# Performance work log

Measured on AMD Instinct MI355X. Metric: run time of the kernel, lower is better.

The kernel has to match this reference:

```python
import jax, jax.numpy as jnp
import numpy as np
import math

H = 512       # hidden_dim
NL = 4        # num_layers
N2 = 32       # d_state // 2
B, L = 8, 4096
DT_MIN, DT_MAX = 1e-3, 1e-1
EPS = 1e-5


def _layer_norm(x, gamma, beta):
    mu = jnp.mean(x, axis=-1, keepdims=True)
    var = jnp.mean(jnp.square(x - mu), axis=-1, keepdims=True)
    return (x - mu) * jax.lax.rsqrt(var + EPS) * gamma + beta


def setup_inputs() -> dict:
    key = jax.random.key(0)
    ks = jax.random.split(key, 8)
    x = jax.random.normal(ks[0], (B, L, H), dtype=jnp.float32)
    # S4DKernel buffers / params, stacked over layers
    log_dt = jax.random.uniform(ks[1], (NL, H)) * (math.log(DT_MAX) - math.log(DT_MIN)) + math.log(DT_MIN)
    A_imag = jnp.broadcast_to(math.pi * jnp.arange(N2, dtype=jnp.float32), (NL, H, N2)).copy()
    log_A_real = jnp.full((NL, H, N2), math.log(0.5), dtype=jnp.float32)
    C = jax.random.normal(ks[2], (NL, H, N2, 2), dtype=jnp.float32)  # view_as_real of cfloat
    D = jax.random.normal(ks[3], (NL, H), dtype=jnp.float32)
    # 1x1 Conv1d h -> 2h (pointwise linear over channels)
    W = jax.random.normal(ks[4], (NL, 2 * H, H), dtype=jnp.float32) / math.sqrt(H)
    b = jax.random.normal(ks[5], (NL, 2 * H), dtype=jnp.float32) * 0.01
    gamma = jnp.ones((NL, H), dtype=jnp.float32)
    beta = jnp.zeros((NL, H), dtype=jnp.float32)
    return dict(x=x, log_dt=log_dt, A_imag=A_imag, log_A_real=log_A_real,
                C=C, D=D, W=W, b=b, gamma=gamma, beta=beta)


def reference(x, log_dt, A_imag, log_A_real, C, D, W, b, gamma, beta):
    Bsz, Lseq, h = x.shape
    t = jnp.arange(Lseq, dtype=jnp.float32)
    for i in range(NL):
        # --- S4D kernel generation ---
        dt = jnp.exp(log_dt[i])                                    # (h,)
        Cc = C[i, ..., 0] + 1j * C[i, ..., 1]                      # (h, n)
        A = -jnp.exp(log_A_real[i]) + 1j * A_imag[i]               # (h, n)
        dA = A * dt[:, None]                                       # (h, n)
        Cmod = Cc * (jnp.exp(dA) - 1.0) / A                        # (h, n)
        # Vandermonde: exp(dA * l), reduced over state dim
        K = 2.0 * jnp.einsum('hn,hnl->hl', Cmod,
                             jnp.exp(dA[:, :, None] * t)).real     # (h, L)
        # --- FFT long convolution ---
        u = jnp.transpose(x, (0, 2, 1))                            # (B, h, L)
        kf = jnp.fft.rfft(K, n=2 * Lseq)                           # (h, L+1)
        uf = jnp.fft.rfft(u, n=2 * Lseq)                           # (B, h, L+1)
        y = jnp.fft.irfft(uf * kf, n=2 * Lseq)[..., :Lseq]         # (B, h, L)
        y = y + u * D[i][:, None]
        y = jax.nn.gelu(y, approximate=False)                      # torch nn.GELU default (erf)
        # 1x1 conv h -> 2h then GLU over channel dim
        z = jnp.einsum('oh,bhl->bol', W[i], y) + b[i][None, :, None]
        a, g = jnp.split(z, 2, axis=1)
        y = a * jax.nn.sigmoid(g)                                  # (B, h, L)
        y = jnp.transpose(y, (0, 2, 1))                            # (B, L, h)
        x = _layer_norm(y + x, gamma[i], beta[i])
    return x
```

## Files before the change

kernel.cpp:

```cpp
#include <hip/hip_runtime.h>
#include <hip/hip_bf16.h>
#include <math.h>

#define H 512
#define NL 4
#define N2 32
#define Bsz 8
#define Lseq 4096
#define BT (Bsz*Lseq)
#define LC2 64
#define NCC (BT/LC2)
#define CPB (Lseq/LC2)

typedef __attribute__((ext_vector_type(8))) short short8;
typedef __attribute__((ext_vector_type(4))) float float4v;


__device__ __forceinline__ float bf2f(unsigned short u) {
    union { unsigned int i; float f; } x; x.i = ((unsigned int)u) << 16; return x.f;
}
__device__ __forceinline__ unsigned short f2bf(float f) {
    union { float f; unsigned int i; } x; x.f = f;
    unsigned int u = x.i + 0x7fff + ((x.i >> 16) & 1);
    return (unsigned short)(u >> 16);
}
__device__ __forceinline__ uint2 pack4bf(float a, float b, float c, float d) {
    uint2 r;
    r.x = (unsigned)f2bf(a) | ((unsigned)f2bf(b) << 16);
    r.y = (unsigned)f2bf(c) | ((unsigned)f2bf(d) << 16);
    return r;
}
__device__ __forceinline__ void async_copy16(const void* g, void* l) {
    __builtin_amdgcn_global_load_lds(
        (const __attribute__((address_space(1))) void*)g,
        (__attribute__((address_space(3))) void*)l, 16, 0, 0);
}

__global__ void wconv_kernel(const float* __restrict__ W, unsigned short* __restrict__ Wbf) {
    int tid = blockIdx.x * 256 + threadIdx.x;
    Wbf[tid] = f2bf(W[tid]);
}

__global__ void params_kernel(const float* __restrict__ log_dt, const float* __restrict__ A_imag,
                              const float* __restrict__ log_A_real, const float* __restrict__ Cin,
                              float* __restrict__ dA, float* __restrict__ Ct) {
    int tid = blockIdx.x * 256 + threadIdx.x;
    int h = tid % H;
    int n = (tid / H) % N2;
    int layer = tid / (H * N2);
    float dt = expf(log_dt[layer * H + h]);
    int pidx = (layer * H + h) * N2 + n;
    float Are = -expf(log_A_real[pidx]);
    float Aim = A_imag[pidx];
    float dre = Are * dt, dim = Aim * dt;
    float er = expf(dre);
    float lre = er * cosf(dim), lim = er * sinf(dim);
    float nre = lre - 1.0f, nim = lim;
    float inv = 1.0f / (Are * Are + Aim * Aim);
    float tre = (nre * Are + nim * Aim) * inv;
    float tim = (nim * Are - nre * Aim) * inv;
    float Ccre = Cin[pidx * 2], Ccim = Cin[pidx * 2 + 1];
    int oidx = ((layer * N2 + n) * 2) * H + h;
    dA[oidx] = dre;  dA[oidx + H] = dim;
    Ct[oidx] = 2.0f * (Ccre * tre - Ccim * tim);
    Ct[oidx + H] = 2.0f * (Ccre * tim + Ccim * tre);
}

__global__ void kergen_k_kernel(const float* __restrict__ dA, const float* __restrict__ Ct,
                                unsigned short* __restrict__ kmat) {
    int t = blockIdx.x * 256 + threadIdx.x;
    int d = t & 63;
    int h = (t >> 6) & (H - 1);
    int layer = t >> 15;
    float fd = (float)d;
    float sum = 0.f;
    for (int n = 0; n < N2; n++) {
        int base = ((layer * N2 + n) * 2) * H + h;
        float dre = dA[base], dim = dA[base + H];
        float Ctr = Ct[base], Cti = Ct[base + H];
        float e = expf(dre * fd);
        sum += Ctr * e * cosf(dim * fd) - Cti * e * sinf(dim * fd);
    }
    kmat[t] = f2bf(sum);
}

__global__ void kergenW_kernel(const float* __restrict__ dA, unsigned short* __restrict__ Wst, int layer) {
    int t = blockIdx.x * 256 + threadIdx.x;
    int j = t & 63;
    int r = (t >> 6) & 63;
    int h = t >> 12;
    int n = r >> 1;
    int base = ((layer * N2 + n) * 2) * H + h;
    float dre = dA[base], dim = dA[base + H];
    float p = (float)(63 - j);
    float e = expf(dre * p);
    Wst[t] = f2bf((r & 1) ? e * sinf(dim * p) : e * cosf(dim * p));
}

__global__ void kergenV_kernel(const float* __restrict__ dA, const float* __restrict__ Ct,
                               unsigned short* __restrict__ Vl, int layer) {
    int t = blockIdx.x * 256 + threadIdx.x;
    int c2 = t & 63;
    int l = (t >> 6) & 63;
    int h = t >> 12;
    int n = c2 >> 1;
    int base = ((layer * N2 + n) * 2) * H + h;
    float dre = dA[base], dim = dA[base + H];
    float Ctr = Ct[base], Cti = Ct[base + H];
    float q = (float)(l + 1);
    float e = expf(dre * q);
    float ar = e * cosf(dim * q), ai = e * sinf(dim * q);
    float vre = Ctr * ar - Cti * ai;
    float vim = Ctr * ai + Cti * ar;
    Vl[t] = f2bf((c2 & 1) ? -vim : vre);
}

__global__ __launch_bounds__(256) void t1_f32_kernel(const float* __restrict__ xi,
                                                     unsigned short* __restrict__ ut) {
    __shared__ float tile[64][68];
    int bx = blockIdx.x;
    int pt = bx & 511, ht = bx >> 9;
    int p0 = pt * 64, h0 = ht * 64;
    int t = threadIdx.x;
    int jr = t & 15, ib = t >> 4;
#pragma unroll
    for (int pass = 0; pass < 4; pass++) {
        int i = ib + pass * 16;
        float4 v = *(const float4*)(xi + (size_t)(p0 + i) * H + h0 + jr * 4);
        tile[i][jr * 4 + 0] = v.x; tile[i][jr * 4 + 1] = v.y;
        tile[i][jr * 4 + 2] = v.z; tile[i][jr * 4 + 3] = v.w;
    }
    __syncthreads();
#pragma unroll
    for (int pass = 0; pass < 4; pass++) {
        int i2 = ib + pass * 16;
        int j2 = jr * 4;
        uint2 pk = pack4bf(tile[j2][i2], tile[j2 + 1][i2], tile[j2 + 2][i2], tile[j2 + 3][i2]);
        *(uint2*)(ut + (size_t)(h0 + i2) * BT + p0 + j2) = pk;
    }
}

__global__ __launch_bounds__(256) void t1_bf16_kernel(const unsigned short* __restrict__ xi,
                                                      unsigned short* __restrict__ ut) {
    __shared__ unsigned short tile[64][72];
    int bx = blockIdx.x;
    int pt = bx & 511, ht = bx >> 9;
    int p0 = pt * 64, h0 = ht * 64;
    int t = threadIdx.x;
    int jr = t & 7, ib = t >> 3;
#pragma unroll
    for (int pass = 0; pass < 2; pass++) {
        int i = ib + pass * 32;
        short8 v = *reinterpret_cast<const short8*>(xi + (size_t)(p0 + i) * H + h0 + jr * 8);
#pragma unroll
        for (int e = 0; e < 8; e++) tile[i][jr * 8 + e] = (unsigned short)v[e];
    }
    __syncthreads();
    int hr = t >> 2, bg = t & 3;
    short8 o0, o1;
#pragma unroll
    for (int r = 0; r < 8; r++) o0[r] = (short)tile[bg * 16 + r][hr];
#pragma unroll
    for (int r = 0; r < 8; r++) o1[r] = (short)tile[bg * 16 + 8 + r][hr];
    unsigned short* dst = ut + (size_t)(h0 + hr) * BT + p0 + bg * 16;
    *reinterpret_cast<short8*>(dst) = o0;
    *reinterpret_cast<short8*>(dst + 8) = o1;
}

__global__ __launch_bounds__(256) void states_kernel(const unsigned short* __restrict__ ut,
                                                     const unsigned short* __restrict__ Wst,
                                                     unsigned short* __restrict__ Sloc) {
    int h = blockIdx.x;
    int wave = threadIdx.x >> 6, lane = threadIdx.x & 63;
    int r16 = lane & 15, quad = lane >> 4;
    const unsigned short* uh = ut + (size_t)h * BT;
    const unsigned short* wh = Wst + (size_t)h * 64 * 64;
    unsigned short* sh = Sloc + (size_t)h * NCC * 64;
    for (int nt = 0; nt < 8; nt++) {
        int cc0 = wave * 128 + nt * 16;
        float4v acc[4] = {};
#pragma unroll
        for (int k0 = 0; k0 < 64; k0 += 32) {
            short8 bf = *reinterpret_cast<const short8*>(uh + (size_t)(cc0 + r16) * 64 + k0 + quad * 8);
#pragma unroll
            for (int mt = 0; mt < 4; mt++) {
                short8 af = *reinterpret_cast<const short8*>(wh + (mt * 16 + r16) * 64 + k0 + quad * 8);
                acc[mt] = __builtin_amdgcn_mfma_f32_16x16x32_bf16(af, bf, acc[mt], 0, 0, 0);
            }
        }
        int cc = cc0 + r16;
#pragma unroll
        for (int mt = 0; mt < 4; mt++) {
            uint2 pk = pack4bf(acc[mt][0], acc[mt][1], acc[mt][2], acc[mt][3]);
            *(uint2*)(sh + (size_t)cc * 64 + mt * 16 + quad * 4) = pk;
        }
    }
}

__global__ void combine_kernel(unsigned short* __restrict__ Sloc, const float* __restrict__ dA, int layer) {
    int t = blockIdx.x * 256 + threadIdx.x;
    int n = t & 31;
    int b = (t >> 5) & 7;
    int h = t >> 8;
    int base = ((layer * N2 + n) * 2) * H + h;
    float dre = dA[base], dim = dA[base + H];
    float e = expf(dre * 64.f);
    float Lr = e * cosf(dim * 64.f), Li = e * sinf(dim * 64.f);
    unsigned int* p = (unsigned int*)Sloc + ((size_t)h * NCC + b * CPB) * 32 + n;
    float sr = 0.f, si = 0.f;
    for (int c = 0; c < CPB; c++) {
        unsigned int v = p[(size_t)c * 32];
        float pr = bf2f(v & 0xffff), pi = bf2f(v >> 16);
        p[(size_t)c * 32] = (unsigned)f2bf(sr) | ((unsigned)f2bf(si) << 16);
        float nr = fmaf(Lr, sr, fmaf(-Li, si, pr));
        float ni = fmaf(Lr, si, fmaf(Li, sr, pi));
        sr = nr; si = ni;
    }
}

__global__ __launch_bounds__(256) void conv_kernel(const unsigned short* __restrict__ ut,
                                                   const unsigned short* __restrict__ kmat,
                                                   const unsigned short* __restrict__ Vl,
                                                   const unsigned short* __restrict__ Sent,
                                                   const float* __restrict__ Dp,
                                                   unsigned short* __restrict__ yt, int layer) {
    __shared__ unsigned short T[64][72];
    int h = blockIdx.x, half = blockIdx.y;
    int t = threadIdx.x;
    const unsigned short* km = kmat + ((size_t)layer * H + h) * 64;
    {
        int l = t >> 2, j0 = (t & 3) * 16;
#pragma unroll
        for (int g = 0; g < 2; g++) {
            short8 v;
#pragma unroll
            for (int e = 0; e < 8; e++) {
                int j = j0 + g * 8 + e;
                v[e] = (j <= l) ? (short)km[l - j] : (short)0;
            }
            *reinterpret_cast<short8*>(&T[l][j0 + g * 8]) = v;
        }
    }
    __syncthreads();
    int wave = t >> 6, lane = t & 63;
    int r16 = lane & 15, quad = lane >> 4;
    const unsigned short* uh = ut + (size_t)h * BT;
    const unsigned short* vh = Vl + (size_t)h * 64 * 64;
    const unsigned short* eh = Sent + (size_t)h * NCC * 64;
    unsigned short* yh = yt + (size_t)h * BT;
    float Dh = Dp[layer * H + h];
    for (int nt = 0; nt < 4; nt++) {
        int cc0 = half * 256 + wave * 64 + nt * 16;
        float4v acc[4] = {};
#pragma unroll
        for (int k0 = 0; k0 < 64; k0 += 32) {
            short8 bf = *reinterpret_cast<const short8*>(uh + (size_t)(cc0 + r16) * 64 + k0 + quad * 8);
#pragma unroll
            for (int mt = 0; mt < 4; mt++) {
                short8 af = *reinterpret_cast<const short8*>(&T[mt * 16 + r16][k0 + quad * 8]);
                acc[mt] = __builtin_amdgcn_mfma_f32_16x16x32_bf16(af, bf, acc[mt], 0, 0, 0);
            }
        }
#pragma unroll
        for (int k0 = 0; k0 < 64; k0 += 32) {
            short8 bf = *reinterpret_cast<const short8*>(eh + (size_t)(cc0 + r16) * 64 + k0 + quad * 8);
#pragma unroll
            for (int mt = 0; mt < 4; mt++) {
                short8 af = *reinterpret_cast<const short8*>(vh + (mt * 16 + r16) * 64 + k0 + quad * 8);
                acc[mt] = __builtin_amdgcn_mfma_f32_16x16x32_bf16(af, bf, acc[mt], 0, 0, 0);
            }
        }
        int cc = cc0 + r16;
#pragma unroll
        for (int mt = 0; mt < 4; mt++) {
            size_t p = (size_t)cc * 64 + mt * 16 + quad * 4;
            ushort4 uu = *(const ushort4*)(uh + p);
            float o[4];
#pragma unroll
            for (int r = 0; r < 4; r++) {
                float y = acc[mt][r] + Dh * bf2f(((const unsigned short*)&uu)[r]);
                o[r] = 0.5f * y * (1.0f + erff(y * 0.70710678118654752f));
            }
            *(uint2*)(yh + p) = pack4bf(o[0], o[1], o[2], o[3]);
        }
    }
}

__global__ __launch_bounds__(256) void transpose2_kernel(const unsigned short* __restrict__ yt,
                                                         unsigned short* __restrict__ yb) {
    __shared__ unsigned short tile[64][72];
    int bx = blockIdx.x;
    int pt = bx & 511, ht = bx >> 9;
    int p0 = pt * 64, h0 = ht * 64;
    int t = threadIdx.x;
    int jr = t & 7, ib = t >> 3;
#pragma unroll
    for (int pass = 0; pass < 2; pass++) {
        int i = ib + pass * 32;
        short8 v = *reinterpret_cast<const short8*>(yt + (size_t)(h0 + i) * BT + p0 + jr * 8);
#pragma unroll
        for (int e = 0; e < 8; e++) tile[i][jr * 8 + e] = (unsigned short)v[e];
    }
    __syncthreads();
    int pp = t >> 2, hg = t & 3;
    short8 o0, o1;
#pragma unroll
    for (int r = 0; r < 8; r++) o0[r] = (short)tile[hg * 16 + r][pp];
#pragma unroll
    for (int r = 0; r < 8; r++) o1[r] = (short)tile[hg * 16 + 8 + r][pp];
    unsigned short* dst = yb + (size_t)(p0 + pp) * H + h0 + hg * 16;
    *reinterpret_cast<short8*>(dst) = o0;
    *reinterpret_cast<short8*>(dst + 8) = o1;
}

__global__ __launch_bounds__(256) void gemm_glu_kernel(const unsigned short* __restrict__ ybf,
                                                       const unsigned short* __restrict__ Wbf,
                                                       const float* __restrict__ bias,
                                                       unsigned short* __restrict__ yo, int layer) {
    __shared__ unsigned short As[128 * 32];
    __shared__ unsigned short Bs[128 * 32];
    int tid = threadIdx.x;
    int wave = tid >> 6, lane = tid & 63;
    int wr = wave >> 1, wc = wave & 1;
    int r16 = lane & 15, quad = lane >> 4;
    int m0 = blockIdx.x * 128;
    int o0 = blockIdx.y * 64;
    const unsigned short* Wl = Wbf + (size_t)layer * 2 * H * H;

    int srow = lane >> 2;
    int scol = ((lane & 3) ^ ((srow >> 1) & 3)) * 8;
    const unsigned short* aSrc0 = ybf + ((size_t)(m0 + wave * 16 + srow)) * H + scol;
    const unsigned short* aSrc1 = aSrc0 + (size_t)64 * H;
    const unsigned short* bSrcA = Wl + ((size_t)(o0 + wave * 16 + srow)) * H + scol;
    const unsigned short* bSrcG = bSrcA + (size_t)512 * H;
    unsigned short* aDst0 = As + (wave * 16) * 32;
    unsigned short* aDst1 = As + (64 + wave * 16) * 32;
    unsigned short* bDstA = Bs + (wave * 16) * 32;
    unsigned short* bDstG = Bs + (64 + wave * 16) * 32;

    int rcol = (quad ^ ((r16 >> 1) & 3)) * 8;

    float4v acc_a[4][2] = {}, acc_g[4][2] = {};

    for (int k0 = 0; k0 < H; k0 += 32) {
        __syncthreads();
        async_copy16(aSrc0, aDst0);
        async_copy16(aSrc1, aDst1);
        async_copy16(bSrcA, bDstA);
        async_copy16(bSrcG, bDstG);
        aSrc0 += 32; aSrc1 += 32; bSrcA += 32; bSrcG += 32;
        __syncthreads();

        short8 af[4], ba[2], bg[2];
#pragma unroll
        for (int mi = 0; mi < 4; mi++)
            af[mi] = *reinterpret_cast<const short8*>(As + (wr * 64 + mi * 16 + r16) * 32 + rcol);
#pragma unroll
        for (int ni = 0; ni < 2; ni++) {
            ba[ni] = *reinterpret_cast<const short8*>(Bs + (wc * 32 + ni * 16 + r16) * 32 + rcol);
            bg[ni] = *reinterpret_cast<const short8*>(Bs + (64 + wc * 32 + ni * 16 + r16) * 32 + rcol);
        }
#pragma unroll
        for (int mi = 0; mi < 4; mi++)
#pragma unroll
            for (int ni = 0; ni < 2; ni++) {
                acc_a[mi][ni] = __builtin_amdgcn_mfma_f32_16x16x32_bf16(af[mi], ba[ni], acc_a[mi][ni], 0, 0, 0);
                acc_g[mi][ni] = __builtin_amdgcn_mfma_f32_16x16x32_bf16(af[mi], bg[ni], acc_g[mi][ni], 0, 0, 0);
            }
    }

    const float* bl = bias + layer * 2 * H;
#pragma unroll
    for (int ni = 0; ni < 2; ni++) {
        int o = o0 + wc * 32 + ni * 16 + r16;
        float ba_ = bl[o], bg_ = bl[H + o];
#pragma unroll
        for (int mi = 0; mi < 4; mi++)
#pragma unroll
            for (int r = 0; r < 4; r++) {
                int l = m0 + wr * 64 + mi * 16 + quad * 4 + r;
                float av = acc_a[mi][ni][r] + ba_;
                float gv = acc_g[mi][ni][r] + bg_;
                yo[(size_t)l * H + o] = f2bf(av * (1.0f / (1.0f + expf(-gv))));
            }
    }
}

__global__ __launch_bounds__(256) void ln_kernel(const unsigned short* __restrict__ yo,
                                                 const float* __restrict__ xf,
                                                 const unsigned short* __restrict__ xb,
                                                 const float* __restrict__ gamma, const float* __restrict__ beta,
                                                 float* __restrict__ of, unsigned short* __restrict__ ob,
                                                 int in_f32, int out_f32, int layer) {
    int wave = threadIdx.x >> 6, lane = threadIdx.x & 63;
    size_t row = (size_t)blockIdx.x * 4 + wave;
    const unsigned short* yp = yo + row * H + lane * 8;
    short8 yv = *reinterpret_cast<const short8*>(yp);
    float v[8];
    if (in_f32) {
        const float* xp = xf + row * H + lane * 8;
        float4 x0 = *(const float4*)(xp);
        float4 x1 = *(const float4*)(xp + 4);
        v[0] = bf2f((unsigned short)yv[0]) + x0.x; v[1] = bf2f((unsigned short)yv[1]) + x0.y;
        v[2] = bf2f((unsigned short)yv[2]) + x0.z; v[3] = bf2f((unsigned short)yv[3]) + x0.w;
        v[4] = bf2f((unsigned short)yv[4]) + x1.x; v[5] = bf2f((unsigned short)yv[5]) + x1.y;
        v[6] = bf2f((unsigned short)yv[6]) + x1.z; v[7] = bf2f((unsigned short)yv[7]) + x1.w;
    } else {
        const unsigned short* xp = xb + row * H + lane * 8;
        short8 xv = *reinterpret_cast<const short8*>(xp);
#pragma unroll
        for (int i = 0; i < 8; i++)
            v[i] = bf2f((unsigned short)yv[i]) + bf2f((unsigned short)xv[i]);
    }
    float s = 0.f, s2 = 0.f;
#pragma unroll
    for (int i = 0; i < 8; i++) { s += v[i]; s2 = fmaf(v[i], v[i], s2); }
#pragma unroll
    for (int off = 32; off; off >>= 1) {
        s += __shfl_xor(s, off);
        s2 += __shfl_xor(s2, off);
    }
    float mu = s * (1.0f / H);
    float var = s2 * (1.0f / H) - mu * mu;
    float inv = rsqrtf(var + 1e-5f);
    const float* gl = gamma + layer * H + lane * 8;
    const float* bl = beta + layer * H + lane * 8;
    float o[8];
#pragma unroll
    for (int i = 0; i < 8; i++)
        o[i] = (v[i] - mu) * inv * gl[i] + bl[i];
    if (out_f32) {
        float* op = of + row * H + lane * 8;
        *(float4*)(op) = make_float4(o[0], o[1], o[2], o[3]);
        *(float4*)(op + 4) = make_float4(o[4], o[5], o[6], o[7]);
    } else {
        unsigned short* op = ob + row * H + lane * 8;
        uint2 p0 = pack4bf(o[0], o[1], o[2], o[3]);
        uint2 p1 = pack4bf(o[4], o[5], o[6], o[7]);
        *(uint2*)(op) = p0;
        *(uint2*)(op + 4) = p1;
    }
}

extern "C" void kernel_launch(void* const* d_in, const int* in_sizes, int n_in,
                              void* d_out, int out_size, void* d_ws, size_t ws_size,
                              hipStream_t stream) {
    const float* x          = (const float*)d_in[0];
    const float* log_dt     = (const float*)d_in[1];
    const float* A_imag     = (const float*)d_in[2];
    const float* log_A_real = (const float*)d_in[3];
    const float* C          = (const float*)d_in[4];
    const float* D          = (const float*)d_in[5];
    const float* W          = (const float*)d_in[6];
    const float* bias       = (const float*)d_in[7];
    const float* gamma      = (const float*)d_in[8];
    const float* beta       = (const float*)d_in[9];

    char* ws = (char*)d_ws;
    unsigned short* xR   = (unsigned short*)(ws + 0);
    unsigned short* Sloc = (unsigned short*)(ws + 67108864);
    unsigned short* u_t  = (unsigned short*)(ws + 100663296);
    unsigned short* ybf  = (unsigned short*)(ws + 100663296);
    unsigned short* y_t  = (unsigned short*)(ws + 134217728);
    unsigned short* yo   = (unsigned short*)(ws + 134217728);
    unsigned short* Wbf  = (unsigned short*)(ws + 167772160);
    unsigned short* WV   = (unsigned short*)(ws + 171966464);
    unsigned short* kmat = (unsigned short*)(ws + 176160768);
    float*          dA   = (float*)(ws + 176422912);
    float*          Ct   = (float*)(ws + 176947200);
    float* xout_final    = (float*)d_out;

    wconv_kernel<<<NL * 2 * H * H / 256, 256, 0, stream>>>(W, Wbf);
    params_kernel<<<NL * N2 * H / 256, 256, 0, stream>>>(log_dt, A_imag, log_A_real, C, dA, Ct);
    kergen_k_kernel<<<NL * H * 64 / 256, 256, 0, stream>>>(dA, Ct, kmat);

    for (int layer = 0; layer < NL; ++layer) {
        if (layer == 0)
            t1_f32_kernel<<<4096, 256, 0, stream>>>(x, u_t);
        else
            t1_bf16_kernel<<<4096, 256, 0, stream>>>(xR, u_t);
        kergenW_kernel<<<H * 64 * 64 / 256, 256, 0, stream>>>(dA, WV, layer);
        states_kernel<<<H, 256, 0, stream>>>(u_t, WV, Sloc);
        combine_kernel<<<H * Bsz * N2 / 256, 256, 0, stream>>>(Sloc, dA, layer);
        kergenV_kernel<<<H * 64 * 64 / 256, 256, 0, stream>>>(dA, Ct, WV, layer);
        conv_kernel<<<dim3(H, 2), 256, 0, stream>>>(u_t, kmat, WV, Sloc, D, y_t, layer);
        transpose2_kernel<<<4096, 256, 0, stream>>>(y_t, ybf);
        gemm_glu_kernel<<<dim3(BT / 128, H / 64), 256, 0, stream>>>(ybf, Wbf, bias, yo, layer);
        int in_f32 = (layer == 0), out_f32 = (layer == NL - 1);
        ln_kernel<<<BT / 4, 256, 0, stream>>>(yo, x, xR, gamma, beta,
                                              xout_final, xR, in_f32, out_f32, layer);
    }
}
```

Measured before the change: 864.2 us.

## Triple-buffer LDS tiles in GEMM-GLU kernel with async prefetch two stages ahead

The GEMM-GLU kernel's K loop now uses three LDS buffers, issuing async global-to-LDS copies two iterations ahead. Explicit vmcnt waits and a single barrier per iteration replace the two syncthreads around each load. This is meant to hide global load latency behind MFMA work. It triples shared memory to 48KB per block, which may lower occupancy, and relies on hand-placed waitcnt counts being correct.

```diff
diff --git a/kernel.cpp b/kernel.cpp
--- a/kernel.cpp
+++ b/kernel.cpp
@@ -317,8 +317,8 @@
                                                        const unsigned short* __restrict__ Wbf,
                                                        const float* __restrict__ bias,
                                                        unsigned short* __restrict__ yo, int layer) {
-    __shared__ unsigned short As[128 * 32];
-    __shared__ unsigned short Bs[128 * 32];
+    __shared__ unsigned short As[3][128 * 32];
+    __shared__ unsigned short Bs[3][128 * 32];
     int tid = threadIdx.x;
     int wave = tid >> 6, lane = tid & 63;
     int wr = wave >> 1, wc = wave & 1;
@@ -329,36 +329,48 @@
 
     int srow = lane >> 2;
     int scol = ((lane & 3) ^ ((srow >> 1) & 3)) * 8;
-    const unsigned short* aSrc0 = ybf + ((size_t)(m0 + wave * 16 + srow)) * H + scol;
-    const unsigned short* aSrc1 = aSrc0 + (size_t)64 * H;
-    const unsigned short* bSrcA = Wl + ((size_t)(o0 + wave * 16 + srow)) * H + scol;
-    const unsigned short* bSrcG = bSrcA + (size_t)512 * H;
-    unsigned short* aDst0 = As + (wave * 16) * 32;
-    unsigned short* aDst1 = As + (64 + wave * 16) * 32;
-    unsigned short* bDstA = Bs + (wave * 16) * 32;
-    unsigned short* bDstG = Bs + (64 + wave * 16) * 32;
+    const unsigned short* aS0 = ybf + ((size_t)(m0 + wave * 16 + srow)) * H + scol;
+    const unsigned short* aS1 = aS0 + (size_t)64 * H;
+    const unsigned short* bSA = Wl + ((size_t)(o0 + wave * 16 + srow)) * H + scol;
+    const unsigned short* bSG = bSA + (size_t)512 * H;
+    const int aoff0 = (wave * 16) * 32;
+    const int aoff1 = (64 + wave * 16) * 32;
 
     int rcol = (quad ^ ((r16 >> 1) & 3)) * 8;
 
     float4v acc_a[4][2] = {}, acc_g[4][2] = {};
 
-    for (int k0 = 0; k0 < H; k0 += 32) {
-        __syncthreads();
-        async_copy16(aSrc0, aDst0);
-        async_copy16(aSrc1, aDst1);
-        async_copy16(bSrcA, bDstA);
-        async_copy16(bSrcG, bDstG);
-        aSrc0 += 32; aSrc1 += 32; bSrcA += 32; bSrcG += 32;
-        __syncthreads();
+    async_copy16(aS0,      &As[0][aoff0]);
+    async_copy16(aS1,      &As[0][aoff1]);
+    async_copy16(bSA,      &Bs[0][aoff0]);
+    async_copy16(bSG,      &Bs[0][aoff1]);
+    async_copy16(aS0 + 32, &As[1][aoff0]);
+    async_copy16(aS1 + 32, &As[1][aoff1]);
+    async_copy16(bSA + 32, &Bs[1][aoff0]);
+    async_copy16(bSG + 32, &Bs[1][aoff1]);
+    asm volatile("s_waitcnt vmcnt(4)" ::: "memory");
+    __builtin_amdgcn_s_barrier();
+
+#pragma unroll
+    for (int ks = 0; ks < 16; ++ks) {
+        const int b = ks % 3;
+        if (ks < 14) {
+            const int nb = (ks + 2) % 3;
+            const int kn = (ks + 2) * 32;
+            async_copy16(aS0 + kn, &As[nb][aoff0]);
+            async_copy16(aS1 + kn, &As[nb][aoff1]);
+            async_copy16(bSA + kn, &Bs[nb][aoff0]);
+            async_copy16(bSG + kn, &Bs[nb][aoff1]);
+        }
 
         short8 af[4], ba[2], bg[2];
 #pragma unroll
         for (int mi = 0; mi < 4; mi++)
-            af[mi] = *reinterpret_cast<const short8*>(As + (wr * 64 + mi * 16 + r16) * 32 + rcol);
+            af[mi] = *reinterpret_cast<const short8*>(&As[b][(wr * 64 + mi * 16 + r16) * 32 + rcol]);
 #pragma unroll
         for (int ni = 0; ni < 2; ni++) {
-            ba[ni] = *reinterpret_cast<const short8*>(Bs + (wc * 32 + ni * 16 + r16) * 32 + rcol);
-            bg[ni] = *reinterpret_cast<const short8*>(Bs + (64 + wc * 32 + ni * 16 + r16) * 32 + rcol);
+            ba[ni] = *reinterpret_cast<const short8*>(&Bs[b][(wc * 32 + ni * 16 + r16) * 32 + rcol]);
+            bg[ni] = *reinterpret_cast<const short8*>(&Bs[b][(64 + wc * 32 + ni * 16 + r16) * 32 + rcol]);
         }
 #pragma unroll
         for (int mi = 0; mi < 4; mi++)
@@ -367,6 +379,14 @@
                 acc_a[mi][ni] = __builtin_amdgcn_mfma_f32_16x16x32_bf16(af[mi], ba[ni], acc_a[mi][ni], 0, 0, 0);
                 acc_g[mi][ni] = __builtin_amdgcn_mfma_f32_16x16x32_bf16(af[mi], bg[ni], acc_g[mi][ni], 0, 0, 0);
             }
+
+        if (ks < 14) {
+            asm volatile("s_waitcnt vmcnt(4) lgkmcnt(0)" ::: "memory");
+            __builtin_amdgcn_s_barrier();
+        } else if (ks == 14) {
+            asm volatile("s_waitcnt vmcnt(0) lgkmcnt(0)" ::: "memory");
+            __builtin_amdgcn_s_barrier();
+        }
     }
 
     const float* bl = bias + layer * 2 * H;
```

New measurement: 854.8 us. Within noise of the previous version (-1.1%).
